# Performance work log

Measured on AMD Instinct MI355X. Metric: run time of the kernel, lower is better.

Reference implementation:

```python
import jax, jax.numpy as jnp
import numpy as np


def setup_inputs() -> dict:
    key = jax.random.key(0)
    ks = jax.random.split(key, 4)
    L, B, T, H, D = 12, 4, 2048, 16, 64
    current_layer = jax.random.normal(ks[0], (B, T, H, D), dtype=jnp.float32)
    all_layers = jax.random.normal(ks[1], (L, B, T, H, D), dtype=jnp.float32)
    # nn.init.normal_(std=0.02) for both projections
    Wq = jax.random.normal(ks[2], (D, D), dtype=jnp.float32) * 0.02
    Wk = jax.random.normal(ks[3], (D, D), dtype=jnp.float32) * 0.02
    scales = jnp.full((L,), 1.0 / L, dtype=jnp.float32)  # LayerScalingFactor init 1/num_layers
    temperature = jnp.ones((1,), dtype=jnp.float32)
    return {
        "current_layer": current_layer,
        "all_layers": all_layers,
        "Wq": Wq,
        "Wk": Wk,
        "scales": scales,
        "temperature": temperature,
        "current_layer_idx": 0,
    }


def reference(current_layer, all_layers, Wq, Wk, scales, temperature, current_layer_idx):
    # current_layer: [B,T,H,D]; all_layers: [L,B,T,H,D] (stack of per-layer outputs)
    # num_heads = 1, so per-head dim == D and scores are over the layer axis L.
    D = current_layer.shape[-1]
    q = jnp.einsum("bthd,ed->bthe", current_layer, Wq)          # query_proj (no bias)
    k = jnp.einsum("lbthd,ed->lbthe", all_layers, Wk)           # key_proj (no bias)
    inv_scale = 1.0 / (jnp.sqrt(jnp.asarray(D, q.dtype)) * jnp.abs(temperature[0]))
    scores = jnp.einsum("bthd,lbthd->bthl", q, k) * inv_scale   # [B,T,H,L]
    attn = jax.nn.softmax(scores, axis=-1)
    attn = attn * scales                                        # per-layer learned scale
    attn = attn / (jnp.sum(attn, axis=-1, keepdims=True) + 1e-6)  # renormalize
    # per-layer accumulation: output += scales[l] * attn[...,l] * all_layers[l]
    out = jnp.einsum("bthl,l,lbthd->bthd", attn, scales, all_layers)
    return out
```

## Files before the change

### kernel.cpp

```cpp
#include <hip/hip_runtime.h>
#include <hip/hip_bf16.h>

constexpr int L = 12;
constexpr int B = 4, T = 2048, H = 16, D = 64;
constexpr int NPOS = B * T * H;
constexpr long long SLAYER = (long long)NPOS * D;
constexpr int PW = 16;
constexpr int NG = 3, GL = 4;

typedef __attribute__((ext_vector_type(8))) short bf16x8;
typedef __attribute__((ext_vector_type(4))) float f32x4;

__device__ __forceinline__ short f2bf(float f) {
  union { __hip_bfloat16 h; short s; } u;
  u.h = __float2bfloat16(f);
  return u.s;
}

__global__ __launch_bounds__(64) void cla_precompute_MT(
    const float* __restrict__ Wq, const float* __restrict__ Wk,
    short* __restrict__ MT) {
  const int n = blockIdx.x;
  const int k = threadIdx.x;
  float acc = 0.f;
  #pragma unroll
  for (int e = 0; e < D; ++e)
    acc = fmaf(Wq[e * D + k], Wk[e * D + n], acc);
  MT[n * D + k] = f2bf(acc);
}

template <int CTRL>
__device__ __forceinline__ float ror_add(float x) {
  int moved = __builtin_amdgcn_update_dpp(0, __float_as_int(x), CTRL, 0xF, 0xF,
                                          false);
  return x + __int_as_float(moved);
}
__device__ __forceinline__ float row_sum16(float x) {
  x = ror_add<0x121>(x);
  x = ror_add<0x122>(x);
  x = ror_add<0x124>(x);
  x = ror_add<0x128>(x);
  return x;
}

__global__ __launch_bounds__(256, 2) void cla_main(
    const float* __restrict__ cur, const float* __restrict__ all,
    const short* __restrict__ MT, const float* __restrict__ scales,
    const float* __restrict__ temperature, float* __restrict__ out) {
  __shared__ float qlds[4][PW * D];

  const int lane = threadIdx.x & 63;
  const int w    = threadIdx.x >> 6;
  const int wid  = blockIdx.x * 4 + w;
  const int pos0 = wid * PW;
  const int ncol = lane & 15;
  const int kq   = lane >> 4;

  const size_t sbase = (size_t)pos0 * D + (size_t)lane * 4;

  float4 yb[2][GL][4];
  #pragma unroll
  for (int i = 0; i < GL; ++i) {
    const float* p = all + (size_t)i * SLAYER + sbase;
    #pragma unroll
    for (int t = 0; t < 4; ++t)
      yb[0][i][t] = *(const float4*)(p + t * 256);
  }

  const float inv_scale = 1.0f / (8.0f * fabsf(temperature[0]));

  bf16x8 af[2];
  {
    const float* xb = cur + (size_t)(pos0 + ncol) * D + kq * 8;
    #pragma unroll
    for (int kc = 0; kc < 2; ++kc) {
      const float4 xlo = *(const float4*)(xb + kc * 32);
      const float4 xhi = *(const float4*)(xb + kc * 32 + 4);
      short a8[8] = {f2bf(xlo.x), f2bf(xlo.y), f2bf(xlo.z), f2bf(xlo.w),
                     f2bf(xhi.x), f2bf(xhi.y), f2bf(xhi.z), f2bf(xhi.w)};
      __builtin_memcpy(&af[kc], a8, 16);
    }
  }
  #pragma unroll
  for (int nt = 0; nt < 4; ++nt) {
    f32x4 acc = {};
    #pragma unroll
    for (int kc = 0; kc < 2; ++kc) {
      const bf16x8 bm =
          *(const bf16x8*)(MT + (nt * 16 + ncol) * D + kc * 32 + kq * 8);
      acc = __builtin_amdgcn_mfma_f32_16x16x32_bf16(af[kc], bm, acc, 0, 0, 0);
    }
    #pragma unroll
    for (int r = 0; r < 4; ++r)
      qlds[w][(4 * kq + r) * D + nt * 16 + ncol] = acc[r] * inv_scale;
  }

  const int gq = lane >> 4;
  const int j  = lane & 15;
  float4 q[4];
  #pragma unroll
  for (int t = 0; t < 4; ++t)
    q[t] = *(const float4*)&qlds[w][(t * 4 + gq) * D + 4 * j];

  float scl[L], scl2[L];
  #pragma unroll
  for (int l = 0; l < L; ++l) {
    scl[l]  = scales[l];
    scl2[l] = scl[l] * scl[l];
  }

  float m[4], S[4], A[4];
  f32x4 N[4];
  #pragma unroll
  for (int t = 0; t < 4; ++t) {
    m[t] = -3.0e38f;
    S[t] = 0.f;
    A[t] = 0.f;
    N[t] = (f32x4){0.f, 0.f, 0.f, 0.f};
  }

  #pragma unroll
  for (int gi = 0; gi < NG; ++gi) {
    if (gi + 1 < NG) {
      #pragma unroll
      for (int i = 0; i < GL; ++i) {
        const float* p = all + (size_t)((gi + 1) * GL + i) * SLAYER + sbase;
        #pragma unroll
        for (int t = 0; t < 4; ++t)
          yb[(gi + 1) & 1][i][t] = *(const float4*)(p + t * 256);
      }
    }

    #pragma unroll
    for (int t = 0; t < 4; ++t) {
      float sc[GL];
      #pragma unroll
      for (int i = 0; i < GL; ++i) {
        const float4 y = yb[gi & 1][i][t];
        const float s =
            q[t].x * y.x + q[t].y * y.y + q[t].z * y.z + q[t].w * y.w;
        sc[i] = row_sum16(s);
      }
      float gm = sc[0];
      #pragma unroll
      for (int i = 1; i < GL; ++i) gm = fmaxf(gm, sc[i]);
      const float mn = fmaxf(m[t], gm);
      const float c  = __expf(m[t] - mn);
      m[t] = mn;

      float e[GL];
      float dS = 0.f, dA = 0.f;
      #pragma unroll
      for (int i = 0; i < GL; ++i) {
        e[i] = __expf(sc[i] - mn);
        dS += e[i];
        dA += scl[gi * GL + i] * e[i];
      }
      S[t] = S[t] * c + dS;
      A[t] = A[t] * c + dA;

      float ax = 0.f, ay = 0.f, az = 0.f, aw = 0.f;
      #pragma unroll
      for (int i = 0; i < GL; ++i) {
        const float wl = scl2[gi * GL + i] * e[i];
        const float4 y = yb[gi & 1][i][t];
        ax = fmaf(wl, y.x, ax);
        ay = fmaf(wl, y.y, ay);
        az = fmaf(wl, y.z, az);
        aw = fmaf(wl, y.w, aw);
      }
      N[t][0] = N[t][0] * c + ax;
      N[t][1] = N[t][1] * c + ay;
      N[t][2] = N[t][2] * c + az;
      N[t][3] = N[t][3] * c + aw;
    }
  }

  #pragma unroll
  for (int t = 0; t < 4; ++t) {
    const float r = 1.0f / (A[t] + 1e-6f * S[t]);
    *(float4*)(out + sbase + t * 256) =
        make_float4(N[t][0] * r, N[t][1] * r, N[t][2] * r, N[t][3] * r);
  }
}

extern "C" void kernel_launch(void* const* d_in, const int* in_sizes, int n_in,
                              void* d_out, int out_size, void* d_ws, size_t ws_size,
                              hipStream_t stream) {
  const float* cur    = (const float*)d_in[0];
  const float* all    = (const float*)d_in[1];
  const float* Wq     = (const float*)d_in[2];
  const float* Wk     = (const float*)d_in[3];
  const float* scales = (const float*)d_in[4];
  const float* temp   = (const float*)d_in[5];
  short* MT = (short*)d_ws;

  cla_precompute_MT<<<64, 64, 0, stream>>>(Wq, Wk, MT);

  const int nwaves  = NPOS / PW;
  const int nblocks = nwaves / 4;
  cla_main<<<nblocks, 256, 0, stream>>>(cur, all, MT, scales, temp,
                                        (float*)d_out);
}
```

Measured before the change: 100.6 us.

## Shrink layer groups, raise occupancy, and use nontemporal loads/stores

Layer groups shrink from 4 to 2 per stage, so the double-buffered prefetch holds fewer layers in registers. The q and scale values are now read from LDS and memory inside the loop instead of being kept in registers. Launch bounds rise to 4 blocks per CU to add waves that hide memory latency. Streaming loads of all_layers and stores of out become nontemporal to avoid cache pollution. The trade-off is a shallower prefetch per wave and extra LDS and scalar loads in the inner loop.

```diff
diff --git a/kernel.cpp b/kernel.cpp
--- a/kernel.cpp
+++ b/kernel.cpp
@@ -6,7 +6,7 @@
 constexpr int NPOS = B * T * H;
 constexpr long long SLAYER = (long long)NPOS * D;
 constexpr int PW = 16;
-constexpr int NG = 3, GL = 4;
+constexpr int NG = 6, GL = 2;
 
 typedef __attribute__((ext_vector_type(8))) short bf16x8;
 typedef __attribute__((ext_vector_type(4))) float f32x4;
@@ -15,6 +15,13 @@
   union { __hip_bfloat16 h; short s; } u;
   u.h = __float2bfloat16(f);
   return u.s;
+}
+
+__device__ __forceinline__ f32x4 ntload4(const float* p) {
+  return __builtin_nontemporal_load((const f32x4*)p);
+}
+__device__ __forceinline__ void ntstore4(float* p, f32x4 v) {
+  __builtin_nontemporal_store(v, (f32x4*)p);
 }
 
 __global__ __launch_bounds__(64) void cla_precompute_MT(
@@ -43,7 +50,7 @@
   return x;
 }
 
-__global__ __launch_bounds__(256, 2) void cla_main(
+__global__ __launch_bounds__(256, 4) void cla_main(
     const float* __restrict__ cur, const float* __restrict__ all,
     const short* __restrict__ MT, const float* __restrict__ scales,
     const float* __restrict__ temperature, float* __restrict__ out) {
@@ -58,19 +65,18 @@
 
   const size_t sbase = (size_t)pos0 * D + (size_t)lane * 4;
 
-  float4 yb[2][GL][4];
+  f32x4 yb[2][GL][4];
   #pragma unroll
   for (int i = 0; i < GL; ++i) {
     const float* p = all + (size_t)i * SLAYER + sbase;
     #pragma unroll
-    for (int t = 0; t < 4; ++t)
-      yb[0][i][t] = *(const float4*)(p + t * 256);
+    for (int t = 0; t < 4; ++t) yb[0][i][t] = ntload4(p + t * 256);
   }
 
   const float inv_scale = 1.0f / (8.0f * fabsf(temperature[0]));
 
-  bf16x8 af[2];
   {
+    bf16x8 af[2];
     const float* xb = cur + (size_t)(pos0 + ncol) * D + kq * 8;
     #pragma unroll
     for (int kc = 0; kc < 2; ++kc) {
@@ -80,34 +86,23 @@
                      f2bf(xhi.x), f2bf(xhi.y), f2bf(xhi.z), f2bf(xhi.w)};
       __builtin_memcpy(&af[kc], a8, 16);
     }
-  }
-  #pragma unroll
-  for (int nt = 0; nt < 4; ++nt) {
-    f32x4 acc = {};
-    #pragma unroll
-    for (int kc = 0; kc < 2; ++kc) {
-      const bf16x8 bm =
-          *(const bf16x8*)(MT + (nt * 16 + ncol) * D + kc * 32 + kq * 8);
-      acc = __builtin_amdgcn_mfma_f32_16x16x32_bf16(af[kc], bm, acc, 0, 0, 0);
-    }
-    #pragma unroll
-    for (int r = 0; r < 4; ++r)
-      qlds[w][(4 * kq + r) * D + nt * 16 + ncol] = acc[r] * inv_scale;
+    #pragma unroll
+    for (int nt = 0; nt < 4; ++nt) {
+      f32x4 acc = {};
+      #pragma unroll
+      for (int kc = 0; kc < 2; ++kc) {
+        const bf16x8 bm =
+            *(const bf16x8*)(MT + (nt * 16 + ncol) * D + kc * 32 + kq * 8);
+        acc = __builtin_amdgcn_mfma_f32_16x16x32_bf16(af[kc], bm, acc, 0, 0, 0);
+      }
+      #pragma unroll
+      for (int r = 0; r < 4; ++r)
+        qlds[w][(4 * kq + r) * D + nt * 16 + ncol] = acc[r] * inv_scale;
+    }
   }
 
   const int gq = lane >> 4;
   const int j  = lane & 15;
-  float4 q[4];
-  #pragma unroll
-  for (int t = 0; t < 4; ++t)
-    q[t] = *(const float4*)&qlds[w][(t * 4 + gq) * D + 4 * j];
-
-  float scl[L], scl2[L];
-  #pragma unroll
-  for (int l = 0; l < L; ++l) {
-    scl[l]  = scales[l];
-    scl2[l] = scl[l] * scl[l];
-  }
 
   float m[4], S[4], A[4];
   f32x4 N[4];
@@ -127,18 +122,19 @@
         const float* p = all + (size_t)((gi + 1) * GL + i) * SLAYER + sbase;
         #pragma unroll
         for (int t = 0; t < 4; ++t)
-          yb[(gi + 1) & 1][i][t] = *(const float4*)(p + t * 256);
+          yb[(gi + 1) & 1][i][t] = ntload4(p + t * 256);
       }
     }
 
     #pragma unroll
     for (int t = 0; t < 4; ++t) {
+      const float4 q = *(const float4*)&qlds[w][(t * 4 + gq) * D + 4 * j];
+
       float sc[GL];
       #pragma unroll
       for (int i = 0; i < GL; ++i) {
-        const float4 y = yb[gi & 1][i][t];
-        const float s =
-            q[t].x * y.x + q[t].y * y.y + q[t].z * y.z + q[t].w * y.w;
+        const f32x4 y = yb[gi & 1][i][t];
+        const float s = q.x * y[0] + q.y * y[1] + q.z * y[2] + q.w * y[3];
         sc[i] = row_sum16(s);
       }
       float gm = sc[0];
@@ -152,9 +148,10 @@
       float dS = 0.f, dA = 0.f;
       #pragma unroll
       for (int i = 0; i < GL; ++i) {
+        const float sl = scales[gi * GL + i];
         e[i] = __expf(sc[i] - mn);
         dS += e[i];
-        dA += scl[gi * GL + i] * e[i];
+        dA += sl * e[i];
       }
       S[t] = S[t] * c + dS;
       A[t] = A[t] * c + dA;
@@ -162,12 +159,13 @@
       float ax = 0.f, ay = 0.f, az = 0.f, aw = 0.f;
       #pragma unroll
       for (int i = 0; i < GL; ++i) {
-        const float wl = scl2[gi * GL + i] * e[i];
-        const float4 y = yb[gi & 1][i][t];
-        ax = fmaf(wl, y.x, ax);
-        ay = fmaf(wl, y.y, ay);
-        az = fmaf(wl, y.z, az);
-        aw = fmaf(wl, y.w, aw);
+        const float sl = scales[gi * GL + i];
+        const float wl = sl * sl * e[i];
+        const f32x4 y = yb[gi & 1][i][t];
+        ax = fmaf(wl, y[0], ax);
+        ay = fmaf(wl, y[1], ay);
+        az = fmaf(wl, y[2], az);
+        aw = fmaf(wl, y[3], aw);
       }
       N[t][0] = N[t][0] * c + ax;
       N[t][1] = N[t][1] * c + ay;
@@ -179,8 +177,12 @@
   #pragma unroll
   for (int t = 0; t < 4; ++t) {
     const float r = 1.0f / (A[t] + 1e-6f * S[t]);
-    *(float4*)(out + sbase + t * 256) =
-        make_float4(N[t][0] * r, N[t][1] * r, N[t][2] * r, N[t][3] * r);
+    f32x4 o;
+    o[0] = N[t][0] * r;
+    o[1] = N[t][1] * r;
+    o[2] = N[t][2] * r;
+    o[3] = N[t][3] * r;
+    ntstore4(out + sbase + t * 256, o);
   }
 }
 
```

New measurement: 155.8 us. +55.0%, slower.
